# Kernel optimization log

Hardware: AMD Instinct MI355X
Metric: run time of the kernel (lower is better)

## Reference

```python
import jax, jax.numpy as jnp
import numpy as np

BS = 8
SP_IN, DN_IN = 256, 128
SP_OUT, DN_OUT = 512, 256
N_STK, N_STK_PNT = 32, 64
COOR = 64
SP_NEAR, DN_NEAR = 2, 10
BN_EPS = 1e-5


def _act(x):
    return jax.nn.leaky_relu(x, 0.2)


def _bn(x, g, b, axes):
    # training-mode batch norm over `axes`, per channel (axis 1)
    m = x.mean(axes, keepdims=True)
    v = x.var(axes, keepdims=True)
    shp = [1] * x.ndim
    shp[1] = x.shape[1]
    return g.reshape(shp) * (x - m) * jax.lax.rsqrt(v + BN_EPS) + b.reshape(shp)


def _conv2d(x, w, b, stride, pad_w):
    # x [B,C,H,W], w [O,I,1,kw]
    y = jax.lax.conv_general_dilated(
        x, w, window_strides=stride, padding=[(0, 0), (pad_w, pad_w)],
        dimension_numbers=('NCHW', 'OIHW', 'NCHW'))
    return y + b[None, :, None, None]


def _sq_dist(a, b):
    # a [B,N,C], b [B,M,C] -> [B,N,M]
    return (jnp.sum(a * a, -1)[:, :, None] + jnp.sum(b * b, -1)[:, None, :]
            - 2.0 * jnp.einsum('bnc,bmc->bnm', a, b))


def _index_points(p, idx):
    # p [B,N,C], idx [B,...] -> [B,...,C]
    B = p.shape[0]
    bidx = jnp.arange(B).reshape((B,) + (1,) * (idx.ndim - 1))
    return p[bidx, idx]


def _fps(x, m):
    # deterministic farthest point sampling, start at index 0. x [B,N,D] -> [B,m]
    B, N, _ = x.shape
    bar = jnp.arange(B)

    def step(carry, _):
        dist, far = carry
        cen = x[bar, far]                       # [B,D]
        d = jnp.sum((x - cen[:, None, :]) ** 2, -1)
        dist = jnp.minimum(dist, d)
        return (dist, jnp.argmax(dist, -1).astype(jnp.int32)), far

    init = (jnp.full((B, N), 1e10, x.dtype), jnp.zeros((B,), jnp.int32))
    _, idx = jax.lax.scan(step, init, None, length=m)
    return idx.T  # [B,m]


def _gcn(x, W, b, g, be, k):
    # DGCNN-style EdgeConv: knn in feature space, edge feat [x_j - x_i, x_i],
    # shared 1x1 conv + BN + act, max over neighbors. x [B,C,N] -> [B,O,N]
    xt = jnp.transpose(x, (0, 2, 1))            # [B,N,C]
    d = _sq_dist(xt, xt)
    _, idx = jax.lax.top_k(-d, k)               # [B,N,k] (includes self)
    neigh = _index_points(xt, idx)              # [B,N,k,C]
    cen = xt[:, :, None, :]
    edge = jnp.concatenate([neigh - cen, jnp.broadcast_to(cen, neigh.shape)], -1)
    h = jnp.einsum('bnkc,oc->bonk', edge, W) + b[None, :, None, None]
    h = _act(_bn(h, g, be, (0, 2, 3)))
    return jnp.max(h, axis=3)                   # [B,O,N]


def _forward(sparse_fea, dense_fea, stk_coor,
             d2s_w, d2s_b, d2s_g, d2s_be,
             gsp_w, gsp_b, gsp_g, gsp_be,
             gdn_w, gdn_b, gdn_g, gdn_be,
             dcv_w, dcv_b, dcv_g, dcv_be):
    bs = sparse_fea.shape[0]
    dn4 = dense_fea.reshape(bs, DN_IN, N_STK, N_STK_PNT)

    # DenseToSparse: conv (1,3) valid, BN, act, max over points -> concat
    h = _act(_bn(_conv2d(dn4, d2s_w, d2s_b, (1, 1), 0), d2s_g, d2s_be, (0, 2, 3)))
    sp_from_dn = jnp.max(h, axis=3)                       # [bs,DN_IN,N_STK]
    union_sparse = jnp.concatenate([sparse_fea, sp_from_dn], 1)

    # SparseToDense: broadcast stroke feature onto its points -> concat
    dn_from_sp = jnp.repeat(sparse_fea[:, :, :, None], N_STK_PNT, axis=3)
    union_dense = jnp.concatenate([dn4, dn_from_sp], 1).reshape(
        bs, SP_IN + DN_IN, N_STK * N_STK_PNT)

    # graph updates
    union_sparse = _gcn(union_sparse, gsp_w, gsp_b, gsp_g, gsp_be, SP_NEAR)   # [bs,SP_OUT,N_STK]
    union_dense = _gcn(union_dense, gdn_w, gdn_b, gdn_g, gdn_be, DN_NEAR)     # [bs,DN_OUT,N_pnt]

    # DownSample: FPS over strokes, gather, strided conv halves point count
    fps_idx = _fps(stk_coor, N_STK // 2)                  # [bs,N_STK//2]
    stk_coor_s = _index_points(stk_coor, fps_idx)         # [bs,N_STK//2,COOR]
    sp = jnp.transpose(_index_points(jnp.transpose(union_sparse, (0, 2, 1)), fps_idx), (0, 2, 1))

    emb_d = union_dense.shape[1]
    dn = union_dense.reshape(bs, emb_d, N_STK, N_STK_PNT).transpose(0, 2, 3, 1)
    dn = dn.reshape(bs, N_STK, N_STK_PNT * emb_d)
    dn = _index_points(dn, fps_idx)                       # gather whole strokes
    dn = dn.reshape(bs, N_STK // 2, N_STK_PNT, emb_d).transpose(0, 3, 1, 2)
    dn = _act(_bn(_conv2d(dn, dcv_w, dcv_b, (1, 2), 1), dcv_g, dcv_be, (0, 2, 3)))
    dn = dn.reshape(bs, dn.shape[1], (N_STK // 2) * (N_STK_PNT // 2))
    return sp, dn, stk_coor_s


def setup_inputs() -> dict:
    key = jax.random.key(0)
    ks = jax.random.split(key, 8)
    C_u = SP_IN + DN_IN

    def rn(k, shape, s=0.05):
        return jax.random.normal(k, shape, jnp.float32) * s

    return {
        'sparse_fea': jax.random.normal(ks[0], (BS, SP_IN, N_STK), jnp.float32),
        'dense_fea': jax.random.normal(ks[1], (BS, DN_IN, N_STK * N_STK_PNT), jnp.float32),
        'stk_coor': jax.random.normal(ks[2], (BS, N_STK, COOR), jnp.float32),
        'd2s_w': rn(ks[3], (DN_IN, DN_IN, 1, 3)), 'd2s_b': jnp.zeros(DN_IN),
        'd2s_g': jnp.ones(DN_IN), 'd2s_be': jnp.zeros(DN_IN),
        'gsp_w': rn(ks[4], (SP_OUT, 2 * C_u)), 'gsp_b': jnp.zeros(SP_OUT),
        'gsp_g': jnp.ones(SP_OUT), 'gsp_be': jnp.zeros(SP_OUT),
        'gdn_w': rn(ks[5], (DN_OUT, 2 * C_u)), 'gdn_b': jnp.zeros(DN_OUT),
        'gdn_g': jnp.ones(DN_OUT), 'gdn_be': jnp.zeros(DN_OUT),
        'dcv_w': rn(ks[6], (DN_OUT, DN_OUT, 1, 3)), 'dcv_b': jnp.zeros(DN_OUT),
        'dcv_g': jnp.ones(DN_OUT), 'dcv_be': jnp.zeros(DN_OUT),
    }


def reference(sparse_fea, dense_fea, stk_coor,
              d2s_w, d2s_b, d2s_g, d2s_be,
              gsp_w, gsp_b, gsp_g, gsp_be,
              gdn_w, gdn_b, gdn_g, gdn_be,
              dcv_w, dcv_b, dcv_g, dcv_be):
    return _forward(sparse_fea, dense_fea, stk_coor,
                    d2s_w, d2s_b, d2s_g, d2s_be,
                    gsp_w, gsp_b, gsp_g, gsp_be,
                    gdn_w, gdn_b, gdn_g, gdn_be,
                    dcv_w, dcv_b, dcv_g, dcv_be)
```

## Files before the change

### kernel.cpp

```cpp
#include <hip/hip_runtime.h>

#define NPTS 2048
#define CUF 384

__device__ __forceinline__ float lrelu(float y){ return y>=0.f ? y : 0.2f*y; }

#define GLD16(g, l) __builtin_amdgcn_global_load_lds( \
    (const __attribute__((address_space(1))) void*)(g), \
    (__attribute__((address_space(3))) void*)(l), 16, 0, 0)

__global__ void k_build_xdn(const float* __restrict__ dense,
                            const float* __restrict__ sparse,
                            float* __restrict__ X){
  int b = blockIdx.y, ch = blockIdx.x;
  int t = threadIdx.x;
  __shared__ float tile[64*128];
  for (int k=0;k<32;k++){
    int f = t + k*256;
    int c = f>>6, j = f&63;
    tile[j*128 + c] = dense[((size_t)b*128 + c)*NPTS + ch*64 + j];
  }
  __syncthreads();
  for (int k=0;k<32;k++){
    int f = t + k*256;
    int j = f>>7, c = f&127;
    X[((size_t)b*NPTS + ch*64 + j)*CUF + c] = tile[f];
  }
  float v = sparse[((size_t)b*256 + t)*32 + ch];
  for (int j=0;j<64;j++) X[((size_t)b*NPTS + ch*64 + j)*CUF + 128 + t] = v;
}

__global__ void k_sn(const float* __restrict__ X, float* __restrict__ sn){
  int g = blockIdx.x*256 + threadIdx.x;
  if (g >= 8*NPTS) return;
  const float* row = X + (size_t)g*CUF;
  float blk[4];
  #pragma unroll
  for (int bI=0;bI<4;bI++){
    const float* p = row + bI*96;
    float r[8];
    #pragma unroll
    for (int l=0;l<8;l++) r[l] = __fmul_rn(p[l], p[l]);
    #pragma unroll 1
    for (int i=8;i<96;i+=8){
      #pragma unroll
      for (int l=0;l<8;l++) r[l] = __fadd_rn(r[l], __fmul_rn(p[i+l], p[i+l]));
    }
    float s01 = __fadd_rn(r[0], r[1]);
    float s23 = __fadd_rn(r[2], r[3]);
    float s45 = __fadd_rn(r[4], r[5]);
    float s67 = __fadd_rn(r[6], r[7]);
    blk[bI] = __fadd_rn(__fadd_rn(s01, s23), __fadd_rn(s45, s67));
  }
  sn[g] = __fadd_rn(__fadd_rn(blk[0], blk[1]), __fadd_rn(blk[2], blk[3]));
}

__global__ __launch_bounds__(256) void k_dist_tri(
    const float* __restrict__ X, float* __restrict__ Dot, int b_base){
  int z = blockIdx.z; int b = b_base + z;
  int t = threadIdx.x;
  int tx = t & 15, ty = t >> 4;
  int idx = blockIdx.x, rb = 0;
  while (idx >= 16 - rb){ idx -= 16 - rb; rb++; }
  int cb = rb + idx;
  __shared__ float U[8448];
  float* Xr = U;
  float* Xc = U + 4096;
  float* Ds = U;
  int r0 = rb*128;
  int c0 = cb*128;
  const size_t xb = (size_t)b*NPTS*CUF;
  const size_t zb = (size_t)z*NPTS*NPTS;

  int wv  = t >> 6;
  int sub = (t & 63) >> 3;
  int gs  = t & 7;
  int rowsA[4]; int swzA[4];
  #pragma unroll
  for (int cc=0;cc<4;cc++){
    int grp = wv*4 + cc;
    int row = grp*8 + sub;
    rowsA[cc] = row;
    swzA[cc] = 4*(gs ^ (row&7));
  }

  float acc[8][8];
  #pragma unroll
  for (int i=0;i<8;i++){
    #pragma unroll
    for (int j=0;j<8;j++) acc[i][j] = 0.f;
  }
  for (int kt=0; kt<12; kt++){
    int k0 = kt*32;
    __syncthreads();
    #pragma unroll
    for (int cc=0;cc<4;cc++){
      int grp = wv*4 + cc;
      GLD16(X + xb + (size_t)(r0+rowsA[cc])*CUF + k0 + swzA[cc], Xr + grp*256);
      GLD16(X + xb + (size_t)(c0+rowsA[cc])*CUF + k0 + swzA[cc], Xc + grp*256);
    }
    __syncthreads();
    #pragma unroll
    for (int kk=0; kk<32; kk+=4){
      int G = kk>>2;
      float4 aa[8], bb[8];
      #pragma unroll
      for (int i=0;i<8;i++){ int r = ty+16*i; aa[i] = *(const float4*)&Xr[r*32 + 4*(G ^ (r&7))]; }
      #pragma unroll
      for (int j=0;j<8;j++){ int r = tx+16*j; bb[j] = *(const float4*)&Xc[r*32 + 4*(G ^ (r&7))]; }
      #pragma unroll
      for (int i=0;i<8;i++){
        #pragma unroll
        for (int j=0;j<8;j++){
          float a_ = acc[i][j];
          a_ = fmaf(aa[i].x, bb[j].x, a_);
          a_ = fmaf(aa[i].y, bb[j].y, a_);
          a_ = fmaf(aa[i].z, bb[j].z, a_);
          a_ = fmaf(aa[i].w, bb[j].w, a_);
          acc[i][j] = a_;
        }
      }
    }
  }
  #pragma unroll
  for (int i=0;i<8;i++){
    size_t rbase = zb + (size_t)(r0 + ty + 16*i)*NPTS + c0;
    #pragma unroll
    for (int j=0;j<8;j++) Dot[rbase + tx + 16*j] = acc[i][j];
  }
  if (rb != cb){
    for (int h=0; h<2; h++){
      __syncthreads();
      #pragma unroll
      for (int i2=0;i2<4;i2++){
        #pragma unroll
        for (int j=0;j<8;j++){
          Ds[(tx+16*j)*65 + ty + 16*i2] = acc[h*4+i2][j];
        }
      }
      __syncthreads();
      for (int e=t; e<128*64; e+=256){
        int col = e>>6, rr = e&63;
        Dot[zb + (size_t)(c0+col)*NPTS + r0 + h*64 + rr] = Ds[col*65 + rr];
      }
    }
  }
}

__global__ __launch_bounds__(256) void k_sel(const float* __restrict__ Dot,
                                             const float* __restrict__ sn,
                                             int* __restrict__ idx, int b_base){
  int t = threadIdx.x;
  int lane = t & 63, w = t >> 6;
  int rglob = blockIdx.x*4 + w;
  int bb = rglob >> 11;
  int r  = rglob & 2047;
  int b  = b_base + bb;
  const float* drow = Dot + ((size_t)bb*NPTS + r)*NPTS;
  const float* snp  = sn + (size_t)b*NPTS;
  float snr = snp[r];
  unsigned long long key[32];
  #pragma unroll
  for (int k=0;k<8;k++){
    int cbase = k*256 + lane*4;
    float4 dd = *(const float4*)&drow[cbase];
    float4 ss = *(const float4*)&snp[cbase];
    float v0 = __fsub_rn(__fadd_rn(snr, ss.x), __fmul_rn(2.0f, dd.x));
    float v1 = __fsub_rn(__fadd_rn(snr, ss.y), __fmul_rn(2.0f, dd.y));
    float v2 = __fsub_rn(__fadd_rn(snr, ss.z), __fmul_rn(2.0f, dd.z));
    float v3 = __fsub_rn(__fadd_rn(snr, ss.w), __fmul_rn(2.0f, dd.w));
    float vv[4] = {v0, v1, v2, v3};
    #pragma unroll
    for (int u=0;u<4;u++){
      unsigned int bits = __float_as_uint(vv[u]);
      unsigned int flip = bits ^ ((unsigned int)((int)bits >> 31) | 0x80000000u);
      key[k*4+u] = ((unsigned long long)flip << 32) | (unsigned int)(cbase + u);
    }
  }
  unsigned long long last = 0ull;
  int out[10];
  #pragma unroll
  for (int q=0;q<10;q++){
    const unsigned long long INF = 0xFFFFFFFFFFFFFFFFull;
    unsigned long long m0[16];
    #pragma unroll
    for (int s=0;s<16;s++){
      unsigned long long a = (key[s]    > last) ? key[s]    : INF;
      unsigned long long c = (key[s+16] > last) ? key[s+16] : INF;
      m0[s] = (c < a) ? c : a;
    }
    #pragma unroll
    for (int s=0;s<8;s++) m0[s] = (m0[s+8] < m0[s]) ? m0[s+8] : m0[s];
    #pragma unroll
    for (int s=0;s<4;s++) m0[s] = (m0[s+4] < m0[s]) ? m0[s+4] : m0[s];
    m0[0] = (m0[2] < m0[0]) ? m0[2] : m0[0];
    m0[1] = (m0[3] < m0[1]) ? m0[3] : m0[1];
    unsigned long long m = (m0[1] < m0[0]) ? m0[1] : m0[0];
    #pragma unroll
    for (int sh=1; sh<64; sh<<=1){
      unsigned long long o = (unsigned long long)__shfl_xor((long long)m, sh, 64);
      m = (o < m) ? o : m;
    }
    last = m;
    out[q] = (int)(m & 0xFFFFFFFFull);
  }
  if (lane == 0){
    int* o = idx + ((size_t)b*NPTS + r)*10;
    #pragma unroll
    for (int q=0;q<10;q++) o[q] = out[q];
  }
}

__global__ void k_prepw(const float* __restrict__ Wsrc, float* __restrict__ Wcat, int Ohalf){
  int g = blockIdx.x*256 + threadIdx.x;
  int total = Ohalf*2*CUF;
  if (g >= total) return;
  int o = g / CUF, c = g % CUF;
  float v;
  if (o < Ohalf) v = Wsrc[(size_t)o*768 + c];
  else { int oo = o - Ohalf; v = Wsrc[(size_t)oo*768 + 384 + c] - Wsrc[(size_t)oo*768 + c]; }
  Wcat[g] = v;
}

__global__ __launch_bounds__(256) void k_gemm_pq2(const float* __restrict__ A, const float* __restrict__ W,
                         const float* __restrict__ bias, float* __restrict__ OUT){
  int b = blockIdx.z, mb = blockIdx.y, ob = blockIdx.x;
  int t = threadIdx.x; int tx = t&15, ty = t>>4;
  __shared__ float Xa[4096];
  __shared__ float Xw[4096];
  int m0 = mb*128, o0 = ob*128;
  float acc[8][8];
  #pragma unroll
  for (int i=0;i<8;i++){
    #pragma unroll
    for (int j=0;j<8;j++) acc[i][j] = 0.f;
  }
  int wv  = t >> 6;
  int sub = (t & 63) >> 3;
  int gs  = t & 7;
  int rowsA[4]; int swzA[4];
  #pragma unroll
  for (int cc=0;cc<4;cc++){
    int grp = wv*4 + cc;
    int row = grp*8 + sub;
    rowsA[cc] = row;
    swzA[cc] = 4*(gs ^ (row&7));
  }
  for (int kt=0; kt<12; kt++){
    int k0 = kt*32;
    __syncthreads();
    #pragma unroll
    for (int cc=0;cc<4;cc++){
      int grp = wv*4 + cc;
      GLD16(A + ((size_t)b*NPTS + m0 + rowsA[cc])*CUF + k0 + swzA[cc], Xa + grp*256);
      GLD16(W + (size_t)(o0 + rowsA[cc])*CUF + k0 + swzA[cc], Xw + grp*256);
    }
    __syncthreads();
    #pragma unroll
    for (int kk=0; kk<32; kk+=4){
      int G = kk>>2;
      float4 aa[8], bb[8];
      #pragma unroll
      for (int i=0;i<8;i++){ int r = ty+16*i; aa[i] = *(const float4*)&Xa[r*32 + 4*(G ^ (r&7))]; }
      #pragma unroll
      for (int j=0;j<8;j++){ int r = tx+16*j; bb[j] = *(const float4*)&Xw[r*32 + 4*(G ^ (r&7))]; }
      #pragma unroll
      for (int i=0;i<8;i++){
        #pragma unroll
        for (int j=0;j<8;j++){
          float a_ = acc[i][j];
          a_ = fmaf(aa[i].x, bb[j].x, a_);
          a_ = fmaf(aa[i].y, bb[j].y, a_);
          a_ = fmaf(aa[i].z, bb[j].z, a_);
          a_ = fmaf(aa[i].w, bb[j].w, a_);
          acc[i][j] = a_;
        }
      }
    }
  }
  #pragma unroll
  for (int i=0;i<8;i++){
    int m = m0 + ty + 16*i;
    #pragma unroll
    for (int j=0;j<8;j++){
      int o = o0 + tx + 16*j;
      float v = acc[i][j];
      if (o >= 256) v += bias[o - 256];
      OUT[((size_t)b*NPTS + m)*512 + o] = v;
    }
  }
}

__global__ __launch_bounds__(256) void k_gemm_pq(const float* __restrict__ A, const float* __restrict__ W,
                         const float* __restrict__ bias,
                         float* __restrict__ OUT, int M, int Ototal, int Ohalf){
  int b = blockIdx.z, mb = blockIdx.y, ob = blockIdx.x;
  int t = threadIdx.x; int tr = t&15, tc = t>>4;
  __shared__ float At[64][68], Wt[64][68];
  int m0 = mb*64, o0 = ob*64;
  float acc[4][4];
  #pragma unroll
  for(int i=0;i<4;i++){
    #pragma unroll
    for(int j=0;j<4;j++) acc[i][j]=0.f;
  }
  int li = t>>2, lk = (t&3)*16;
  for (int kt=0;kt<6;kt++){
    int k0 = kt*64;
    {
      int m = m0 + li;
      if (m < M){
        const float4* p = (const float4*)(A + ((size_t)b*M + m)*CUF + k0 + lk);
        #pragma unroll
        for (int e=0;e<4;e++) *(float4*)&At[li][lk+e*4] = p[e];
      } else {
        float4 z = make_float4(0.f,0.f,0.f,0.f);
        #pragma unroll
        for (int e=0;e<4;e++) *(float4*)&At[li][lk+e*4] = z;
      }
      const float4* pw = (const float4*)(W + (size_t)(o0+li)*CUF + k0 + lk);
      #pragma unroll
      for (int e=0;e<4;e++) *(float4*)&Wt[li][lk+e*4] = pw[e];
    }
    __syncthreads();
    #pragma unroll
    for (int k4=0;k4<16;k4++){
      float4 aa[4], bb[4];
      aa[0] = *(const float4*)&At[tr   ][k4*4];
      aa[1] = *(const float4*)&At[tr+16][k4*4];
      aa[2] = *(const float4*)&At[tr+32][k4*4];
      aa[3] = *(const float4*)&At[tr+48][k4*4];
      bb[0] = *(const float4*)&Wt[tc   ][k4*4];
      bb[1] = *(const float4*)&Wt[tc+16][k4*4];
      bb[2] = *(const float4*)&Wt[tc+32][k4*4];
      bb[3] = *(const float4*)&Wt[tc+48][k4*4];
      #pragma unroll
      for(int i=0;i<4;i++){
        #pragma unroll
        for(int j=0;j<4;j++)
          acc[i][j] += aa[i].x*bb[j].x + aa[i].y*bb[j].y + aa[i].z*bb[j].z + aa[i].w*bb[j].w;
      }
    }
    __syncthreads();
  }
  #pragma unroll
  for(int i=0;i<4;i++){
    int m = m0 + tr + 16*i;
    if (m < M){
      #pragma unroll
      for(int j=0;j<4;j++){
        int o = o0 + tc + 16*j;
        float v = acc[i][j];
        if (o >= Ohalf) v += bias[o - Ohalf];
        OUT[((size_t)b*M + m)*Ototal + o] = v;
      }
    }
  }
}

__global__ __launch_bounds__(256) void k_gather_dn(const float* __restrict__ PQ, const int* __restrict__ idx,
                            float* __restrict__ dmax, float* __restrict__ dmin, double* __restrict__ part){
  int b = blockIdx.y, nb = blockIdx.x; int t = threadIdx.x;
  __shared__ int sidx[640];
  int n0 = nb*64;
  for (int k=t; k<640; k+=256) sidx[k] = idx[((size_t)b*NPTS + n0)*10 + k] & 2047;
  __syncthreads();
  double s=0.0, s2=0.0;
  const size_t pb = (size_t)b*NPTS*512;
  for (int n=0;n<64;n++){
    float qv = PQ[pb + (size_t)(n0+n)*512 + 256 + t];
    float mx = -3.4e38f, mn = 3.4e38f;
    #pragma unroll
    for (int k=0;k<10;k++){
      int m = sidx[n*10+k];
      float h = PQ[pb + (size_t)m*512 + t] + qv;
      mx = fmaxf(mx,h); mn = fminf(mn,h);
      s += h; s2 += (double)h*(double)h;
    }
    dmax[((size_t)b*NPTS + n0+n)*256 + t] = mx;
    dmin[((size_t)b*NPTS + n0+n)*256 + t] = mn;
  }
  size_t blk = (size_t)b*32 + nb;
  part[(blk*256 + t)*2] = s; part[(blk*256 + t)*2+1] = s2;
}

__global__ void k_reduce(const double* __restrict__ part, float* __restrict__ mv,
                         int nblk, int C, int count){
  int c = blockIdx.x; int t = threadIdx.x;
  double s=0.0, s2=0.0;
  for (int k=t;k<nblk;k+=64){ s += part[((size_t)k*C+c)*2]; s2 += part[((size_t)k*C+c)*2+1]; }
  #pragma unroll
  for (int off=32; off>=1; off>>=1){ s += __shfl_down(s, off, 64); s2 += __shfl_down(s2, off, 64); }
  if (t==0){
    double mean = s / (double)count;
    double var = s2 / (double)count - mean*mean;
    mv[c*2] = (float)mean;
    mv[c*2+1] = (float)(1.0 / sqrt(var + 1e-5));
  }
}

__global__ void k_epi(const float* __restrict__ xmin, float* __restrict__ xmax,
                      const float* __restrict__ mv, const float* __restrict__ g,
                      const float* __restrict__ be, int C, size_t total){
  size_t i = (size_t)blockIdx.x*256 + threadIdx.x;
  if (i>=total) return;
  int c = (int)(i % (size_t)C);
  float gg = g[c];
  float x = gg >= 0.f ? xmax[i] : xmin[i];
  float y = gg*(x - mv[c*2])*mv[c*2+1] + be[c];
  xmax[i] = lrelu(y);
}

__global__ __launch_bounds__(128) void k_d2s(const float* __restrict__ dense,
                      const float* __restrict__ w, const float* __restrict__ bias,
                      float* __restrict__ mx, float* __restrict__ mn, double* __restrict__ part){
  int b = blockIdx.y, s = blockIdx.x; int t = threadIdx.x;
  __shared__ float IN[128*64];
  for (int k=0;k<64;k++){
    int f = t + k*128;
    int ci = f>>6, wj = f&63;
    IN[f] = dense[((size_t)b*128 + ci)*NPTS + s*64 + wj];
  }
  __syncthreads();
  float acc[62];
  float bv = bias[t];
  #pragma unroll
  for (int wj=0;wj<62;wj++) acc[wj]=bv;
  for (int ci=0;ci<128;ci++){
    const float* wp = w + ((size_t)t*128 + ci)*3;
    float w0 = wp[0], w1 = wp[1], w2 = wp[2];
    const float* row = &IN[ci*64];
    #pragma unroll
    for (int wj=0;wj<62;wj++) acc[wj] += row[wj]*w0 + row[wj+1]*w1 + row[wj+2]*w2;
  }
  float vmx=-3.4e38f, vmn=3.4e38f; double ss=0.0, ss2=0.0;
  #pragma unroll
  for (int wj=0;wj<62;wj++){ float v = acc[wj]; vmx=fmaxf(vmx,v); vmn=fminf(vmn,v); ss+=v; ss2+=(double)v*(double)v; }
  mx[((size_t)b*32+s)*128 + t] = vmx;
  mn[((size_t)b*32+s)*128 + t] = vmn;
  part[(((size_t)b*32+s)*128 + t)*2] = ss; part[(((size_t)b*32+s)*128 + t)*2+1] = ss2;
}

__global__ void k_build_xs(const float* __restrict__ sparse,
                           const float* __restrict__ mx, const float* __restrict__ mn,
                           const float* __restrict__ mv, const float* __restrict__ g,
                           const float* __restrict__ be, float* __restrict__ Xs){
  int b = blockIdx.x; int c = threadIdx.x;
  for (int n=0;n<32;n++){
    float v;
    if (c < 256) v = sparse[((size_t)b*256 + c)*32 + n];
    else {
      int cc = c-256;
      float gg = g[cc];
      float x = gg>=0.f ? mx[((size_t)b*32+n)*128+cc] : mn[((size_t)b*32+n)*128+cc];
      v = lrelu(gg*(x - mv[cc*2])*mv[cc*2+1] + be[cc]);
    }
    Xs[((size_t)b*32+n)*384 + c] = v;
  }
}

__global__ __launch_bounds__(256) void k_knn_sp(const float* __restrict__ Xs, int* __restrict__ idx){
  int b = blockIdx.x; int t = threadIdx.x;
  __shared__ float Xh[32*388];
  __shared__ float snl[32];
  __shared__ float D[32*33];
  for (int k=t;k<32*384;k+=256){ int n=k/384, c=k-n*384; Xh[n*388+c] = Xs[(size_t)b*32*384 + k]; }
  __syncthreads();
  if (t<32){ double s=0.0; for (int c=0;c<384;c++){ double v=(double)Xh[t*388+c]; s+=v*v; } snl[t]=(float)s; }
  __syncthreads();
  for (int p=t;p<1024;p+=256){
    int n=p>>5, m=p&31;
    const float* A=&Xh[n*388]; const float* B=&Xh[m*388];
    double s=0.0;
    for (int c=0;c<384;c++) s += (double)A[c]*(double)B[c];
    D[n*33+m] = (float)((double)snl[m] - 2.0*s);
  }
  __syncthreads();
  if (t<32){
    float v0=3.4e38f,v1=3.4e38f; int i0=0,i1=0;
    for (int m=0;m<32;m++){
      float v=D[t*33+m];
      if (v < v0){ v1=v0;i1=i0; v0=v;i0=m; }
      else if (v < v1){ v1=v;i1=m; }
    }
    idx[((size_t)b*32+t)*2]=i0; idx[((size_t)b*32+t)*2+1]=i1;
  }
}

__global__ void k_gather_sp(const float* __restrict__ PQ, const int* __restrict__ idx,
                            float* __restrict__ umax, float* __restrict__ umin, double* __restrict__ part){
  int b = blockIdx.x; int t = threadIdx.x;
  double s=0.0, s2=0.0;
  for (int n=0;n<32;n++){
    float qv = PQ[((size_t)b*32+n)*1024 + 512 + t];
    float mxv=-3.4e38f, mnv=3.4e38f;
    #pragma unroll
    for (int k=0;k<2;k++){
      int m = idx[((size_t)b*32+n)*2+k] & 31;
      float h = PQ[((size_t)b*32+m)*1024 + t] + qv;
      mxv=fmaxf(mxv,h); mnv=fminf(mnv,h); s+=h; s2+=(double)h*(double)h;
    }
    umax[((size_t)b*32+n)*512+t]=mxv; umin[((size_t)b*32+n)*512+t]=mnv;
  }
  part[((size_t)b*512+t)*2]=s; part[((size_t)b*512+t)*2+1]=s2;
}

__global__ void k_fps(const float* __restrict__ coor, int* __restrict__ fps){
  int b = blockIdx.x; int t = threadIdx.x;
  __shared__ float C[32*64]; __shared__ float dist[32]; __shared__ int fs;
  for (int k=t;k<2048;k+=64) C[k] = coor[(size_t)b*2048 + k];
  if (t<32) dist[t]=1e10f;
  if (t==0) fs=0;
  __syncthreads();
  for (int it=0; it<16; it++){
    int f = fs;
    if (t==0) fps[b*16+it] = f;
    if (t<32){
      float d=0.f;
      for (int c=0;c<64;c++){ float df = C[t*64+c]-C[f*64+c]; d += df*df; }
      dist[t] = fminf(dist[t], d);
    }
    __syncthreads();
    if (t==0){
      float bd=-1.f; int bi=0;
      for (int n=0;n<32;n++){ if (dist[n]>bd){bd=dist[n];bi=n;} }
      fs=bi;
    }
    __syncthreads();
  }
}

__global__ void k_out0(const float* __restrict__ usp, const int* __restrict__ fps, float* __restrict__ out0){
  int b = blockIdx.y, s = blockIdx.x; int t = threadIdx.x;
  int n = fps[b*16+s] & 31;
  out0[((size_t)b*512 + t)*16 + s] = usp[((size_t)b*32+n)*512 + t];
}
__global__ void k_out2(const float* __restrict__ coor, const int* __restrict__ fps, float* __restrict__ out2){
  int b = blockIdx.x; int t = threadIdx.x;
  for (int e=t; e<1024; e+=256){
    int s=e>>6, c=e&63;
    out2[(size_t)b*1024 + e] = coor[((size_t)b*32 + (fps[b*16+s]&31))*64 + c];
  }
}

__global__ __launch_bounds__(256) void k_dcv(const float* __restrict__ gdn, const int* __restrict__ fps,
                      const float* __restrict__ w, const float* __restrict__ bias,
                      float* __restrict__ pre, double* __restrict__ part){
  int b = blockIdx.y, s = blockIdx.x; int t = threadIdx.x;
  __shared__ float I[64*128];
  int n0 = (fps[b*16+s] & 31)*64;
  const size_t gbase = ((size_t)b*NPTS + n0)*256;
  float acc[32];
  float bv = bias[t];
  #pragma unroll
  for (int q=0;q<32;q++) acc[q]=bv;
  for (int half=0; half<2; half++){
    int cbase = half*128;
    __syncthreads();
    for (int e=t; e<8192; e+=256){
      int p = e>>7, c = e&127;
      I[e] = gdn[gbase + (size_t)p*256 + cbase + c];
    }
    __syncthreads();
    for (int ci=0; ci<128; ci+=4){
      float wv[4][3];
      const float* wp = w + ((size_t)t*256 + cbase + ci)*3;
      #pragma unroll
      for (int q=0;q<4;q++){ wv[q][0]=wp[q*3]; wv[q][1]=wp[q*3+1]; wv[q][2]=wp[q*3+2]; }
      #pragma unroll
      for (int q=0;q<32;q++){
        float4 ev = *(const float4*)&I[(2*q)*128 + ci];
        acc[q] += ev.x*wv[0][1] + ev.y*wv[1][1] + ev.z*wv[2][1] + ev.w*wv[3][1];
        float4 ov = *(const float4*)&I[(2*q+1)*128 + ci];
        acc[q] += ov.x*wv[0][2] + ov.y*wv[1][2] + ov.z*wv[2][2] + ov.w*wv[3][2];
        if (q < 31) acc[q+1] += ov.x*wv[0][0] + ov.y*wv[1][0] + ov.z*wv[2][0] + ov.w*wv[3][0];
      }
    }
  }
  double ss=0.0, ss2=0.0;
  #pragma unroll
  for (int q=0;q<32;q++){ ss += acc[q]; ss2 += (double)acc[q]*(double)acc[q]; }
  float* o = pre + (((size_t)b*256 + t)*16 + s)*32;
  #pragma unroll
  for (int q=0;q<32;q++) o[q] = acc[q];
  part[(((size_t)b*16+s)*256 + t)*2] = ss; part[(((size_t)b*16+s)*256 + t)*2+1] = ss2;
}

__global__ void k_epi_dcv(const float* __restrict__ pre, const float* __restrict__ mv,
                          const float* __restrict__ g, const float* __restrict__ be,
                          float* __restrict__ out1){
  size_t i = (size_t)blockIdx.x*256 + threadIdx.x;
  int c = (int)((i>>9) & 255);
  float gg = g[c];
  float y = gg*(pre[i]-mv[c*2])*mv[c*2+1] + be[c];
  out1[i] = lrelu(y);
}

extern "C" void kernel_launch(void* const* d_in, const int* in_sizes, int n_in,
                              void* d_out, int out_size, void* d_ws, size_t ws_size,
                              hipStream_t stream){
  const float* sparse = (const float*)d_in[0];
  const float* dense  = (const float*)d_in[1];
  const float* coor   = (const float*)d_in[2];
  const float* d2s_w  = (const float*)d_in[3];
  const float* d2s_b  = (const float*)d_in[4];
  const float* d2s_g  = (const float*)d_in[5];
  const float* d2s_be = (const float*)d_in[6];
  const float* gsp_w  = (const float*)d_in[7];
  const float* gsp_b  = (const float*)d_in[8];
  const float* gsp_g  = (const float*)d_in[9];
  const float* gsp_be = (const float*)d_in[10];
  const float* gdn_w  = (const float*)d_in[11];
  const float* gdn_b  = (const float*)d_in[12];
  const float* gdn_g  = (const float*)d_in[13];
  const float* gdn_be = (const float*)d_in[14];
  const float* dcv_w  = (const float*)d_in[15];
  const float* dcv_b  = (const float*)d_in[16];
  const float* dcv_g  = (const float*)d_in[17];
  const float* dcv_be = (const float*)d_in[18];

  float* out0 = (float*)d_out;
  float* out1 = out0 + 8*512*16;
  float* out2 = out1 + (size_t)8*256*512;

  char* base = (char*)d_ws; size_t off = 0;
  auto alloc = [&](size_t bytes)->void*{ void* p = base + off; off += (bytes + 255) & ~(size_t)255; return p; };
  float* Xdn  = (float*)alloc((size_t)8*2048*384*4);
  float* sn   = (float*)alloc((size_t)8*2048*4);
  int*   idxd = (int*)alloc((size_t)8*2048*10*4);
  float* PQ   = (float*)alloc((size_t)8*2048*512*4);
  float* dmax = (float*)alloc((size_t)8*2048*256*4);
  float* dmin = (float*)alloc((size_t)8*2048*256*4);
  double* partdn = (double*)alloc((size_t)256*256*2*8);
  float* mvdn = (float*)alloc(256*2*4);
  float* Wcd  = (float*)alloc((size_t)512*384*4);
  float* Wcs  = (float*)alloc((size_t)1024*384*4);
  float* Xs   = (float*)alloc((size_t)8*32*384*4);
  int*   idxs = (int*)alloc(8*32*2*4);
  float* PQs  = (float*)alloc((size_t)8*32*1024*4);
  float* umax = (float*)alloc((size_t)8*32*512*4);
  float* umin = (float*)alloc((size_t)8*32*512*4);
  double* partsp = (double*)alloc((size_t)8*512*2*8);
  float* mvsp = (float*)alloc(512*2*4);
  float* d2mx = (float*)alloc((size_t)8*32*128*4);
  float* d2mn = (float*)alloc((size_t)8*32*128*4);
  double* partd2 = (double*)alloc((size_t)256*128*2*8);
  float* mvd2 = (float*)alloc(128*2*4);
  int* fps = (int*)alloc(8*16*4);
  float* dcvpre = (float*)alloc((size_t)8*256*512*4);
  double* partdcv = (double*)alloc((size_t)128*256*2*8);
  float* mvdcv = (float*)alloc(256*2*4);
  if (off > ws_size) return;

  float* Dot = PQ;

  k_build_xdn<<<dim3(32,8), 256, 0, stream>>>(dense, sparse, Xdn);
  k_sn<<<64, 256, 0, stream>>>(Xdn, sn);
  k_dist_tri<<<dim3(136,1,4), 256, 0, stream>>>(Xdn, Dot, 0);
  k_sel<<<2048, 256, 0, stream>>>(Dot, sn, idxd, 0);
  k_dist_tri<<<dim3(136,1,4), 256, 0, stream>>>(Xdn, Dot, 4);
  k_sel<<<2048, 256, 0, stream>>>(Dot, sn, idxd, 4);
  k_prepw<<<768, 256, 0, stream>>>(gdn_w, Wcd, 256);
  k_prepw<<<1536, 256, 0, stream>>>(gsp_w, Wcs, 512);
  k_gemm_pq2<<<dim3(4,16,8), 256, 0, stream>>>(Xdn, Wcd, gdn_b, PQ);
  k_gather_dn<<<dim3(32,8), 256, 0, stream>>>(PQ, idxd, dmax, dmin, partdn);
  k_reduce<<<256, 64, 0, stream>>>(partdn, mvdn, 256, 256, 163840);
  k_epi<<<16384, 256, 0, stream>>>(dmin, dmax, mvdn, gdn_g, gdn_be, 256, (size_t)8*2048*256);
  k_d2s<<<dim3(32,8), 128, 0, stream>>>(dense, d2s_w, d2s_b, d2mx, d2mn, partd2);
  k_reduce<<<128, 64, 0, stream>>>(partd2, mvd2, 256, 128, 15872);
  k_build_xs<<<8, 384, 0, stream>>>(sparse, d2mx, d2mn, mvd2, d2s_g, d2s_be, Xs);
  k_knn_sp<<<8, 256, 0, stream>>>(Xs, idxs);
  k_gemm_pq<<<dim3(16,1,8), 256, 0, stream>>>(Xs, Wcs, gsp_b, PQs, 32, 1024, 512);
  k_gather_sp<<<8, 512, 0, stream>>>(PQs, idxs, umax, umin, partsp);
  k_reduce<<<512, 64, 0, stream>>>(partsp, mvsp, 8, 512, 512);
  k_epi<<<512, 256, 0, stream>>>(umin, umax, mvsp, gsp_g, gsp_be, 512, (size_t)8*32*512);
  k_fps<<<8, 64, 0, stream>>>(coor, fps);
  k_out0<<<dim3(16,8), 512, 0, stream>>>(umax, fps, out0);
  k_out2<<<8, 256, 0, stream>>>(coor, fps, out2);
  k_dcv<<<dim3(16,8), 256, 0, stream>>>(dmax, fps, dcv_w, dcv_b, dcvpre, partdcv);
  k_reduce<<<256, 64, 0, stream>>>(partdcv, mvdcv, 128, 256, 4096);
  k_epi_dcv<<<4096, 256, 0, stream>>>(dcvpre, mvdcv, dcv_g, dcv_be, out1);
}
```

Baseline: 835.8 us.

## Split dense conv kernel across output-position groups for more parallelism

```diff
diff --git a/kernel.cpp b/kernel.cpp
--- a/kernel.cpp
+++ b/kernel.cpp
@@ -546,44 +546,43 @@
 __global__ __launch_bounds__(256) void k_dcv(const float* __restrict__ gdn, const int* __restrict__ fps,
                       const float* __restrict__ w, const float* __restrict__ bias,
                       float* __restrict__ pre, double* __restrict__ part){
-  int b = blockIdx.y, s = blockIdx.x; int t = threadIdx.x;
-  __shared__ float I[64*128];
+  int s = blockIdx.x, qg = blockIdx.y, b = blockIdx.z; int t = threadIdx.x;
+  __shared__ float I[17*256];
   int n0 = (fps[b*16+s] & 31)*64;
   const size_t gbase = ((size_t)b*NPTS + n0)*256;
-  float acc[32];
+  for (int e=t; e<17*256; e+=256){
+    int lp = e>>8, c = e&255;
+    int p = 16*qg - 1 + lp;
+    I[e] = (p >= 0) ? gdn[gbase + (size_t)p*256 + c] : 0.f;
+  }
+  __syncthreads();
+  float acc[8];
   float bv = bias[t];
   #pragma unroll
-  for (int q=0;q<32;q++) acc[q]=bv;
-  for (int half=0; half<2; half++){
-    int cbase = half*128;
-    __syncthreads();
-    for (int e=t; e<8192; e+=256){
-      int p = e>>7, c = e&127;
-      I[e] = gdn[gbase + (size_t)p*256 + cbase + c];
-    }
-    __syncthreads();
-    for (int ci=0; ci<128; ci+=4){
-      float wv[4][3];
-      const float* wp = w + ((size_t)t*256 + cbase + ci)*3;
-      #pragma unroll
-      for (int q=0;q<4;q++){ wv[q][0]=wp[q*3]; wv[q][1]=wp[q*3+1]; wv[q][2]=wp[q*3+2]; }
-      #pragma unroll
-      for (int q=0;q<32;q++){
-        float4 ev = *(const float4*)&I[(2*q)*128 + ci];
-        acc[q] += ev.x*wv[0][1] + ev.y*wv[1][1] + ev.z*wv[2][1] + ev.w*wv[3][1];
-        float4 ov = *(const float4*)&I[(2*q+1)*128 + ci];
-        acc[q] += ov.x*wv[0][2] + ov.y*wv[1][2] + ov.z*wv[2][2] + ov.w*wv[3][2];
-        if (q < 31) acc[q+1] += ov.x*wv[0][0] + ov.y*wv[1][0] + ov.z*wv[2][0] + ov.w*wv[3][0];
-      }
+  for (int q=0;q<8;q++) acc[q]=bv;
+  for (int ci=0; ci<256; ci+=4){
+    float wv[4][3];
+    const float* wp = w + ((size_t)t*256 + ci)*3;
+    #pragma unroll
+    for (int u=0;u<4;u++){ wv[u][0]=wp[u*3]; wv[u][1]=wp[u*3+1]; wv[u][2]=wp[u*3+2]; }
+    #pragma unroll
+    for (int q=0;q<8;q++){
+      float4 a0 = *(const float4*)&I[(2*q  )*256 + ci];
+      float4 a1 = *(const float4*)&I[(2*q+1)*256 + ci];
+      float4 a2 = *(const float4*)&I[(2*q+2)*256 + ci];
+      acc[q] += a0.x*wv[0][0] + a0.y*wv[1][0] + a0.z*wv[2][0] + a0.w*wv[3][0];
+      acc[q] += a1.x*wv[0][1] + a1.y*wv[1][1] + a1.z*wv[2][1] + a1.w*wv[3][1];
+      acc[q] += a2.x*wv[0][2] + a2.y*wv[1][2] + a2.z*wv[2][2] + a2.w*wv[3][2];
     }
   }
   double ss=0.0, ss2=0.0;
   #pragma unroll
-  for (int q=0;q<32;q++){ ss += acc[q]; ss2 += (double)acc[q]*(double)acc[q]; }
-  float* o = pre + (((size_t)b*256 + t)*16 + s)*32;
-  #pragma unroll
-  for (int q=0;q<32;q++) o[q] = acc[q];
-  part[(((size_t)b*16+s)*256 + t)*2] = ss; part[(((size_t)b*16+s)*256 + t)*2+1] = ss2;
+  for (int q=0;q<8;q++){ ss += acc[q]; ss2 += (double)acc[q]*(double)acc[q]; }
+  float* o = pre + (((size_t)b*256 + t)*16 + s)*32 + qg*8;
+  #pragma unroll
+  for (int q=0;q<8;q++) o[q] = acc[q];
+  size_t blk = ((size_t)b*16 + s)*4 + qg;
+  part[(blk*256 + t)*2] = ss; part[(blk*256 + t)*2+1] = ss2;
 }
 
 __global__ void k_epi_dcv(const float* __restrict__ pre, const float* __restrict__ mv,
@@ -648,7 +647,7 @@
   float* mvd2 = (float*)alloc(128*2*4);
   int* fps = (int*)alloc(8*16*4);
   float* dcvpre = (float*)alloc((size_t)8*256*512*4);
-  double* partdcv = (double*)alloc((size_t)128*256*2*8);
+  double* partdcv = (double*)alloc((size_t)512*256*2*8);
   float* mvdcv = (float*)alloc(256*2*4);
   if (off > ws_size) return;
 
@@ -677,7 +676,7 @@
   k_fps<<<8, 64, 0, stream>>>(coor, fps);
   k_out0<<<dim3(16,8), 512, 0, stream>>>(umax, fps, out0);
   k_out2<<<8, 256, 0, stream>>>(coor, fps, out2);
-  k_dcv<<<dim3(16,8), 256, 0, stream>>>(dmax, fps, dcv_w, dcv_b, dcvpre, partdcv);
-  k_reduce<<<256, 64, 0, stream>>>(partdcv, mvdcv, 128, 256, 4096);
+  k_dcv<<<dim3(16,4,8), 256, 0, stream>>>(dmax, fps, dcv_w, dcv_b, dcvpre, partdcv);
+  k_reduce<<<256, 64, 0, stream>>>(partdcv, mvdcv, 512, 256, 4096);
   k_epi_dcv<<<4096, 256, 0, stream>>>(dcvpre, mvdcv, dcv_g, dcv_be, out1);
 }
```

Measured after the change: 760.2 us. 9.1% less time.
